# Kernel tuning notes

Measured on AMD Instinct MI355X. Metric: run time of the kernel, lower is better.

The kernel has to match this reference:

```python
import jax, jax.numpy as jnp
import numpy as np

NUM_HEADS = 16
KEY_DIM = 64
NUM_FEATURES = 256
D_MODEL = NUM_HEADS * KEY_DIM
EPS = 1e-6


def softmax_kernel(data, proj):
    # data: [..., N, D], proj: [D, F]
    # Faithful to source: ratio uses proj.shape[0] (=D), matching the TF code.
    data_normalizer = 1.0 / jnp.sqrt(jnp.sqrt(jnp.asarray(data.shape[-1], data.dtype)))
    ratio = 1.0 / jnp.sqrt(jnp.asarray(proj.shape[0], data.dtype))
    data = data_normalizer * data
    data_dash = jnp.einsum('...nd,df->...nf', data, proj)
    diag = jnp.sum(jnp.square(data), axis=-1, keepdims=True)  # [..., N, 1]
    return ratio * (jnp.exp(data_dash - diag / 2.0) + EPS)


def setup_inputs() -> dict:
    key = jax.random.key(0)
    ks = jax.random.split(key, 12)
    B, N = 4, 4096
    s = 1.0 / np.sqrt(D_MODEL)
    inp = {
        'queries': jax.random.normal(ks[0], (B, N, D_MODEL), jnp.float32),
        'keys': jax.random.normal(ks[1], (B, N, D_MODEL), jnp.float32),
        'Wq': jax.random.normal(ks[2], (D_MODEL, D_MODEL), jnp.float32) * s,
        'bq': jnp.zeros((D_MODEL,), jnp.float32),
        'Wk': jax.random.normal(ks[3], (D_MODEL, D_MODEL), jnp.float32) * s,
        'bk': jnp.zeros((D_MODEL,), jnp.float32),
        'Wv': jax.random.normal(ks[4], (D_MODEL, D_MODEL), jnp.float32) * s,
        'bv': jnp.zeros((D_MODEL,), jnp.float32),
        'Wo': jax.random.normal(ks[5], (D_MODEL, D_MODEL), jnp.float32) * s,
        'bo': jnp.zeros((D_MODEL,), jnp.float32),
        # GlorotNormal for [KEY_DIM, NUM_FEATURES]
        'proj': jax.random.normal(ks[6], (KEY_DIM, NUM_FEATURES), jnp.float32)
                * np.sqrt(2.0 / (KEY_DIM + NUM_FEATURES)),
    }
    return inp


def reference(queries, keys, Wq, bq, Wk, bk, Wv, bv, Wo, bo, proj):
    # Original code uses x = queries for q, k, v (self-attention); keys arg unused.
    x = queries
    B, N, _ = x.shape
    H, D = NUM_HEADS, KEY_DIM

    def split_heads(t):
        return t.reshape(B, N, H, D).transpose(0, 2, 1, 3)  # [B,H,N,D]

    q = split_heads(x @ Wq + bq)
    k = split_heads(x @ Wk + bk)
    v = split_heads(x @ Wv + bv)

    q_prime = softmax_kernel(q, proj)  # [B,H,N,F]
    k_prime = softmax_kernel(k, proj)  # [B,H,N,F]

    kv = jnp.einsum('bhnf,bhnd->bhfd', k_prime, v)        # [B,H,F,D]
    qkv = jnp.einsum('bhnf,bhfd->bhnd', q_prime, kv)       # [B,H,N,D]
    k_sum = jnp.sum(k_prime, axis=2)                        # [B,H,F]
    norm = jnp.einsum('bhnf,bhf->bhn', q_prime, k_sum) + EPS
    qkv = qkv / norm[..., None]

    out = qkv.transpose(0, 2, 1, 3).reshape(B, N, H * D)    # [B,N,d_model]
    return out @ Wo + bo
```

## Files before the change

### kernel.cpp

```cpp
#include <hip/hip_runtime.h>

typedef __attribute__((ext_vector_type(8))) short short8;
typedef __attribute__((ext_vector_type(4))) float f32x4;

#define MFMA16 __builtin_amdgcn_mfma_f32_16x16x32_bf16

#define GLOAD16(gp, lp) __builtin_amdgcn_global_load_lds(                      \
    (const __attribute__((address_space(1))) void*)(gp),                       \
    (__attribute__((address_space(3))) void*)(lp), 16, 0, 0)

__device__ __forceinline__ unsigned short f2bf(float f) {
  unsigned int u = __float_as_uint(f);
  unsigned int r = u + 0x7fffu + ((u >> 16) & 1u);
  return (unsigned short)(r >> 16);
}
__device__ __forceinline__ float bf2f(unsigned short h) {
  return __uint_as_float(((unsigned int)h) << 16);
}

__global__ __launch_bounds__(256) void cast_x_kernel(
    const float* __restrict__ in, unsigned short* __restrict__ out, int n4) {
  int i = blockIdx.x * 256 + threadIdx.x;
  if (i >= n4) return;
  float4 v = reinterpret_cast<const float4*>(in)[i];
  ushort4 o;
  o.x = f2bf(v.x); o.y = f2bf(v.y); o.z = f2bf(v.z); o.w = f2bf(v.w);
  reinterpret_cast<ushort4*>(out)[i] = o;
}

__global__ __launch_bounds__(256) void tcast_f32_kernel(
    const float* __restrict__ in, unsigned short* __restrict__ out, int R, int C) {
  __shared__ float t[64][65];
  int c0 = blockIdx.x * 64, r0 = blockIdx.y * 64;
  int tx = threadIdx.x, ty = threadIdx.y;
#pragma unroll
  for (int i = 0; i < 16; ++i)
    t[ty + 4 * i][tx] = in[(size_t)(r0 + ty + 4 * i) * C + c0 + tx];
  __syncthreads();
#pragma unroll
  for (int i = 0; i < 16; ++i)
    out[(size_t)(c0 + ty + 4 * i) * R + r0 + tx] = f2bf(t[tx][ty + 4 * i]);
}

__global__ __launch_bounds__(256) void tcast4_kernel(
    const float* __restrict__ i0, const float* __restrict__ i1,
    const float* __restrict__ i2, const float* __restrict__ i3,
    unsigned short* __restrict__ o0, unsigned short* __restrict__ o1,
    unsigned short* __restrict__ o2, unsigned short* __restrict__ o3) {
  const float* in = i0; unsigned short* out = o0;
  if (blockIdx.z == 1) { in = i1; out = o1; }
  else if (blockIdx.z == 2) { in = i2; out = o2; }
  else if (blockIdx.z == 3) { in = i3; out = o3; }
  __shared__ float t[64][65];
  int c0 = blockIdx.x * 64, r0 = blockIdx.y * 64;
  int tx = threadIdx.x, ty = threadIdx.y;
#pragma unroll
  for (int i = 0; i < 16; ++i)
    t[ty + 4 * i][tx] = in[(size_t)(r0 + ty + 4 * i) * 1024 + c0 + tx];
  __syncthreads();
#pragma unroll
  for (int i = 0; i < 16; ++i)
    out[(size_t)(c0 + ty + 4 * i) * 1024 + r0 + tx] = f2bf(t[tx][ty + 4 * i]);
}

template <int OUTF>
__global__ __launch_bounds__(256) void gemm_bt_kernel(
    const unsigned short* __restrict__ A,
    const unsigned short* W0, const unsigned short* W1, const unsigned short* W2,
    const float* b0, const float* b1, const float* b2,
    void* o0, void* o1, void* o2) {
  constexpr int KD = 1024, ND = 1024;
  const unsigned short* W = W0; const float* bias = b0; void* op = o0;
  if (blockIdx.z == 1) { W = W1; bias = b1; op = o1; }
  else if (blockIdx.z == 2) { W = W2; bias = b2; op = o2; }

  __shared__ unsigned short lsA[128 * 32];
  __shared__ unsigned short lsB[128 * 32];
  extern __shared__ unsigned short tt[];
  int tid = threadIdx.x;
  int w = tid >> 6, lane = tid & 63;
  int m0 = blockIdx.x * 128, n0 = blockIdx.y * 128;
  int wm = (w >> 1) * 64, wn = (w & 1) * 64;

  int srow0 = (w * 2 + 0) * 16 + (lane >> 2);
  int srow1 = (w * 2 + 1) * 16 + (lane >> 2);
  int scol = (lane & 3) * 8;
  const unsigned short* gA0 = A + (size_t)(m0 + srow0) * KD + scol;
  const unsigned short* gA1 = A + (size_t)(m0 + srow1) * KD + scol;
  const unsigned short* gB0 = W + (size_t)(n0 + srow0) * KD + scol;
  const unsigned short* gB1 = W + (size_t)(n0 + srow1) * KD + scol;
  unsigned short* lA0 = &lsA[(w * 2 + 0) * 512];
  unsigned short* lA1 = &lsA[(w * 2 + 1) * 512];
  unsigned short* lB0 = &lsB[(w * 2 + 0) * 512];
  unsigned short* lB1 = &lsB[(w * 2 + 1) * 512];

  f32x4 acc[4][4];
#pragma unroll
  for (int fm = 0; fm < 4; ++fm)
#pragma unroll
    for (int fn = 0; fn < 4; ++fn) acc[fm][fn] = (f32x4){0.f, 0.f, 0.f, 0.f};

  for (int kt = 0; kt < KD; kt += 32) {
    GLOAD16(gA0 + kt, lA0);
    GLOAD16(gA1 + kt, lA1);
    GLOAD16(gB0 + kt, lB0);
    GLOAD16(gB1 + kt, lB1);
    __syncthreads();
    short8 af[4], bfr[4];
#pragma unroll
    for (int fm = 0; fm < 4; ++fm)
      af[fm] = *reinterpret_cast<const short8*>(
          &lsA[(wm + fm * 16 + (lane & 15)) * 32 + (lane >> 4) * 8]);
#pragma unroll
    for (int fn = 0; fn < 4; ++fn)
      bfr[fn] = *reinterpret_cast<const short8*>(
          &lsB[(wn + fn * 16 + (lane & 15)) * 32 + (lane >> 4) * 8]);
#pragma unroll
    for (int fm = 0; fm < 4; ++fm)
#pragma unroll
      for (int fn = 0; fn < 4; ++fn)
        acc[fm][fn] = MFMA16(af[fm], bfr[fn], acc[fm][fn], 0, 0, 0);
    __syncthreads();
  }

  bool vpath = (OUTF == 3) && (blockIdx.z == 2);
#pragma unroll
  for (int fn = 0; fn < 4; ++fn) {
    int coll = wn + fn * 16 + (lane & 15);
    float bv = bias[n0 + coll];
#pragma unroll
    for (int fm = 0; fm < 4; ++fm) {
#pragma unroll
      for (int j = 0; j < 4; ++j) {
        int rowl = wm + fm * 16 + (lane >> 4) * 4 + j;
        float v = acc[fm][fn][j] + bv;
        if constexpr (OUTF == 1) {
          reinterpret_cast<float*>(op)[(size_t)(m0 + rowl) * ND + n0 + coll] = v;
        } else {
          if (vpath)
            tt[coll * 136 + rowl] = f2bf(v);
          else
            reinterpret_cast<unsigned short*>(op)[(size_t)(m0 + rowl) * ND + n0 + coll] =
                f2bf(v);
        }
      }
    }
  }
  if constexpr (OUTF == 3) {
    if (vpath) {
      __syncthreads();
      int b = m0 >> 12, tok0 = m0 & 4095;
      int c = tid >> 1, half = (tid & 1) * 64;
      unsigned short* dst = reinterpret_cast<unsigned short*>(op) +
                            (size_t)(b * 1024 + n0 + c) * 4096 + tok0 + half;
#pragma unroll
      for (int i = 0; i < 8; ++i) {
        short8 vv = *reinterpret_cast<const short8*>(&tt[c * 136 + half + i * 8]);
        *reinterpret_cast<short8*>(dst + i * 8) = vv;
      }
    }
  }
}

__global__ __launch_bounds__(256) void kv_fused_kernel(
    const unsigned short* __restrict__ K, const unsigned short* __restrict__ PT,
    const unsigned short* __restrict__ VT,
    float* __restrict__ kvp, float* __restrict__ ksp) {
  __shared__ unsigned short kp[256 * 40];
  int s = blockIdx.x, bh = blockIdx.y, b = bh >> 4, h = bh & 15;
  int tid = threadIdx.x, w = tid >> 6, lane = tid & 63;
  int lo = lane & 15, hi = lane >> 4;
  int f0w = w * 64;

  short8 pb[4][2];
#pragma unroll
  for (int fn = 0; fn < 4; ++fn) {
    int f = f0w + fn * 16 + lo;
    pb[fn][0] = *reinterpret_cast<const short8*>(PT + (size_t)f * 64 + hi * 8);
    pb[fn][1] = *reinterpret_cast<const short8*>(PT + (size_t)f * 64 + 32 + hi * 8);
  }
  const unsigned short* vbase[4];
#pragma unroll
  for (int fn = 0; fn < 4; ++fn)
    vbase[fn] = VT + (size_t)(bh * 64 + fn * 16 + lo) * 4096;

  f32x4 acck[4][4];
#pragma unroll
  for (int fm = 0; fm < 4; ++fm)
#pragma unroll
    for (int fn = 0; fn < 4; ++fn) acck[fm][fn] = (f32x4){0.f, 0.f, 0.f, 0.f};
  float ks[4] = {0.f, 0.f, 0.f, 0.f};

  for (int c = 0; c < 16; ++c) {
    int n0 = s * 512 + c * 32;
    const unsigned short* Ab = K + (size_t)(b * 4096 + n0) * 1024 + h * 64;
    short8 af[2][2], b2[4];
#pragma unroll
    for (int fm = 0; fm < 2; ++fm)
#pragma unroll
      for (int kt = 0; kt < 2; ++kt)
        af[fm][kt] = *reinterpret_cast<const short8*>(
            Ab + (size_t)(fm * 16 + lo) * 1024 + kt * 32 + hi * 8);
#pragma unroll
    for (int fn = 0; fn < 4; ++fn)
      b2[fn] = *reinterpret_cast<const short8*>(vbase[fn] + n0 + hi * 8);

    float dp[2] = {0.f, 0.f};
#pragma unroll
    for (int fm = 0; fm < 2; ++fm)
#pragma unroll
      for (int kt = 0; kt < 2; ++kt)
#pragma unroll
        for (int j = 0; j < 8; ++j) {
          float qv = bf2f((unsigned short)af[fm][kt][j]);
          dp[fm] += qv * qv;
        }
#pragma unroll
    for (int fm = 0; fm < 2; ++fm) {
      dp[fm] += __shfl_xor(dp[fm], 16);
      dp[fm] += __shfl_xor(dp[fm], 32);
    }
    f32x4 accf[2][4];
#pragma unroll
    for (int fm = 0; fm < 2; ++fm)
#pragma unroll
      for (int fn = 0; fn < 4; ++fn) accf[fm][fn] = (f32x4){0.f, 0.f, 0.f, 0.f};
#pragma unroll
    for (int fn = 0; fn < 4; ++fn) {
      accf[0][fn] = MFMA16(af[0][0], pb[fn][0], accf[0][fn], 0, 0, 0);
      accf[0][fn] = MFMA16(af[0][1], pb[fn][1], accf[0][fn], 0, 0, 0);
      accf[1][fn] = MFMA16(af[1][0], pb[fn][0], accf[1][fn], 0, 0, 0);
      accf[1][fn] = MFMA16(af[1][1], pb[fn][1], accf[1][fn], 0, 0, 0);
    }
#pragma unroll
    for (int fm = 0; fm < 2; ++fm)
#pragma unroll
      for (int fn = 0; fn < 4; ++fn) {
        ushort4 pk;
#pragma unroll
        for (int j = 0; j < 4; ++j) {
          float dg = __shfl(dp[fm], hi * 4 + j);
          float v = 0.125f *
                    (__expf(0.35355339059327373f * accf[fm][fn][j] - 0.0625f * dg) + 1e-6f);
          ks[fn] += v;
          ((unsigned short*)&pk)[j] = f2bf(v);
        }
        *reinterpret_cast<ushort4*>(&kp[(f0w + fn * 16 + lo) * 40 + fm * 16 + hi * 4]) = pk;
      }
    short8 a2[4];
#pragma unroll
    for (int fm = 0; fm < 4; ++fm)
      a2[fm] = *reinterpret_cast<const short8*>(&kp[(f0w + fm * 16 + lo) * 40 + hi * 8]);
#pragma unroll
    for (int fm = 0; fm < 4; ++fm)
#pragma unroll
      for (int fn = 0; fn < 4; ++fn)
        acck[fm][fn] = MFMA16(a2[fm], b2[fn], acck[fm][fn], 0, 0, 0);
  }
#pragma unroll
  for (int fn = 0; fn < 4; ++fn) {
    float v = ks[fn];
    v += __shfl_xor(v, 16);
    v += __shfl_xor(v, 32);
    if (hi == 0)
      ksp[(size_t)(s * 64 + bh) * 256 + f0w + fn * 16 + lo] = v;
  }
#pragma unroll
  for (int fm = 0; fm < 4; ++fm)
#pragma unroll
    for (int fn = 0; fn < 4; ++fn)
#pragma unroll
      for (int j = 0; j < 4; ++j)
        kvp[((size_t)(s * 64 + bh) * 256 + f0w + fm * 16 + hi * 4 + j) * 64 + fn * 16 + lo] =
            acck[fm][fn][j];
}

__global__ __launch_bounds__(256) void kvred_kernel(
    const float* __restrict__ kvp, const float* __restrict__ ksp,
    unsigned short* __restrict__ kvT, float* __restrict__ ksum) {
  __shared__ float t[64][65];
  int bh = blockIdx.x, g = blockIdx.y, tid = threadIdx.x;
  int fbase = g * 64;
  int fo = tid >> 2, dq = (tid & 3) * 16;
  float sum[16];
#pragma unroll
  for (int i = 0; i < 16; ++i) sum[i] = 0.f;
#pragma unroll
  for (int s = 0; s < 8; ++s) {
    const float* base = kvp + ((size_t)(s * 64 + bh) * 256 + fbase + fo) * 64 + dq;
#pragma unroll
    for (int i = 0; i < 16; ++i) sum[i] += base[i];
  }
#pragma unroll
  for (int i = 0; i < 16; ++i) t[fo][dq + i] = sum[i];
  __syncthreads();
  int d = tid >> 2, fq = (tid & 3) * 16;
  unsigned short wv[16];
#pragma unroll
  for (int i = 0; i < 16; ++i) wv[i] = f2bf(t[fq + i][d]);
  unsigned short* dst = kvT + (size_t)(bh * 64 + d) * 256 + fbase + fq;
  *reinterpret_cast<short8*>(dst) = *reinterpret_cast<const short8*>(&wv[0]);
  *reinterpret_cast<short8*>(dst + 8) = *reinterpret_cast<const short8*>(&wv[8]);
  if (g == 0) {
    float tsum = 0.f;
#pragma unroll
    for (int s = 0; s < 8; ++s) tsum += ksp[(size_t)(s * 64 + bh) * 256 + tid];
    ksum[bh * 256 + tid] = tsum;
  }
}

__global__ __launch_bounds__(256) void qkv_fused_kernel(
    const unsigned short* __restrict__ Q, const unsigned short* __restrict__ PT,
    const unsigned short* __restrict__ KVT, const float* __restrict__ KSUM,
    unsigned short* __restrict__ Y) {
  __shared__ unsigned short qp[128 * 128];
  int bh = blockIdx.y, b = bh >> 4, h = bh & 15;
  int t0 = blockIdx.x * 128;
  int tid = threadIdx.x, w = tid >> 6, lane = tid & 63;
  int lo = lane & 15, hi = lane >> 4;
  int r0 = w * 32;
  const unsigned short* Ab = Q + (size_t)(b * 4096 + t0 + r0) * 1024 + h * 64;

  float ksr[16];
#pragma unroll
  for (int fn = 0; fn < 16; ++fn) ksr[fn] = KSUM[bh * 256 + fn * 16 + lo];

  short8 af[2][2];
  float dp[2] = {0.f, 0.f};
#pragma unroll
  for (int fm = 0; fm < 2; ++fm)
#pragma unroll
    for (int kt = 0; kt < 2; ++kt) {
      af[fm][kt] = *reinterpret_cast<const short8*>(
          Ab + (size_t)(fm * 16 + lo) * 1024 + kt * 32 + hi * 8);
#pragma unroll
      for (int j = 0; j < 8; ++j) {
        float qv = bf2f((unsigned short)af[fm][kt][j]);
        dp[fm] += qv * qv;
      }
    }
#pragma unroll
  for (int fm = 0; fm < 2; ++fm) {
    dp[fm] += __shfl_xor(dp[fm], 16);
    dp[fm] += __shfl_xor(dp[fm], 32);
  }

  float np[2][4] = {{0.f, 0.f, 0.f, 0.f}, {0.f, 0.f, 0.f, 0.f}};
  f32x4 acco[2][4];
#pragma unroll
  for (int fm = 0; fm < 2; ++fm)
#pragma unroll
    for (int fn = 0; fn < 4; ++fn) acco[fm][fn] = (f32x4){0.f, 0.f, 0.f, 0.f};

#pragma unroll
  for (int hf = 0; hf < 2; ++hf) {
    f32x4 accf[2][8];
#pragma unroll
    for (int fm = 0; fm < 2; ++fm)
#pragma unroll
      for (int fn = 0; fn < 8; ++fn) accf[fm][fn] = (f32x4){0.f, 0.f, 0.f, 0.f};
#pragma unroll
    for (int fn = 0; fn < 8; ++fn) {
      int f = hf * 128 + fn * 16 + lo;
      short8 pb0 = *reinterpret_cast<const short8*>(PT + (size_t)f * 64 + hi * 8);
      short8 pb1 = *reinterpret_cast<const short8*>(PT + (size_t)f * 64 + 32 + hi * 8);
      accf[0][fn] = MFMA16(af[0][0], pb0, accf[0][fn], 0, 0, 0);
      accf[0][fn] = MFMA16(af[0][1], pb1, accf[0][fn], 0, 0, 0);
      accf[1][fn] = MFMA16(af[1][0], pb0, accf[1][fn], 0, 0, 0);
      accf[1][fn] = MFMA16(af[1][1], pb1, accf[1][fn], 0, 0, 0);
    }
#pragma unroll
    for (int fm = 0; fm < 2; ++fm)
#pragma unroll
      for (int fn = 0; fn < 8; ++fn)
#pragma unroll
        for (int j = 0; j < 4; ++j) {
          float dg = __shfl(dp[fm], hi * 4 + j);
          float v = 0.125f *
                    (__expf(0.35355339059327373f * accf[fm][fn][j] - 0.0625f * dg) + 1e-6f);
          np[fm][j] += v * ksr[hf * 8 + fn];
          int row = r0 + fm * 16 + hi * 4 + j;
          int fl = fn * 16 + lo;
          int byt = (row * 256 + fl * 2) ^ ((row & 7) << 4);
          *reinterpret_cast<unsigned short*>(reinterpret_cast<char*>(qp) + byt) = f2bf(v);
        }
#pragma unroll
    for (int kt2 = 0; kt2 < 4; ++kt2) {
      short8 a2[2], b2[4];
#pragma unroll
      for (int fm = 0; fm < 2; ++fm) {
        int row = r0 + fm * 16 + lo;
        int byt = (row * 256 + kt2 * 64 + hi * 16) ^ ((row & 7) << 4);
        a2[fm] = *reinterpret_cast<const short8*>(reinterpret_cast<char*>(qp) + byt);
      }
#pragma unroll
      for (int fn = 0; fn < 4; ++fn)
        b2[fn] = *reinterpret_cast<const short8*>(
            KVT + (size_t)(bh * 64 + fn * 16 + lo) * 256 + hf * 128 + kt2 * 32 + hi * 8);
#pragma unroll
      for (int fm = 0; fm < 2; ++fm)
#pragma unroll
        for (int fn = 0; fn < 4; ++fn)
          acco[fm][fn] = MFMA16(a2[fm], b2[fn], acco[fm][fn], 0, 0, 0);
    }
  }
#pragma unroll
  for (int fm = 0; fm < 2; ++fm)
#pragma unroll
    for (int j = 0; j < 4; ++j) {
      np[fm][j] += __shfl_xor(np[fm][j], 1);
      np[fm][j] += __shfl_xor(np[fm][j], 2);
      np[fm][j] += __shfl_xor(np[fm][j], 4);
      np[fm][j] += __shfl_xor(np[fm][j], 8);
    }
#pragma unroll
  for (int fm = 0; fm < 2; ++fm)
#pragma unroll
    for (int j = 0; j < 4; ++j) {
      float nv = np[fm][j] + 1e-6f;
      int row = b * 4096 + t0 + r0 + fm * 16 + hi * 4 + j;
#pragma unroll
      for (int fn = 0; fn < 4; ++fn)
        Y[(size_t)row * 1024 + h * 64 + fn * 16 + lo] = f2bf(acco[fm][fn][j] / nv);
    }
}

extern "C" void kernel_launch(void* const* d_in, const int* in_sizes, int n_in,
                              void* d_out, int out_size, void* d_ws, size_t ws_size,
                              hipStream_t stream) {
  (void)in_sizes; (void)n_in; (void)out_size; (void)ws_size;
  const float* x    = (const float*)d_in[0];
  const float* Wq   = (const float*)d_in[2];
  const float* bq   = (const float*)d_in[3];
  const float* Wk   = (const float*)d_in[4];
  const float* bk   = (const float*)d_in[5];
  const float* Wv   = (const float*)d_in[6];
  const float* bv   = (const float*)d_in[7];
  const float* Wo   = (const float*)d_in[8];
  const float* bo   = (const float*)d_in[9];
  const float* proj = (const float*)d_in[10];
  float* out = (float*)d_out;

  constexpr size_t SZ_XB = (size_t)16384 * 1024 * 2;
  constexpr size_t SZ_W  = (size_t)1024 * 1024 * 2;
  constexpr size_t SZ_PT = (size_t)256 * 64 * 2;

  char* p = (char*)d_ws;
  size_t off = 0;
  char* a_xb  = p + off; off += SZ_XB;
  char* a_WqT = p + off; off += SZ_W;
  char* a_WkT = p + off; off += SZ_W;
  char* a_WvT = p + off; off += SZ_W;
  char* a_WoT = p + off; off += SZ_W;
  char* a_pT  = p + off; off += SZ_PT;
  char* a_qb  = p + off; off += SZ_XB;
  char* a_kb  = p + off; off += SZ_XB;
  char* a_ksp  = p + off; off += (size_t)8 * 64 * 256 * 4;
  char* a_kvT  = p + off; off += (size_t)64 * 64 * 256 * 2;
  char* a_ksum = p + off; off += (size_t)64 * 256 * 4;

  char* a_kvp = a_xb;
  char* a_vT = (char*)d_out;
  char* a_y = a_kb;

  dim3 tb(64, 4);

  cast_x_kernel<<<16384, 256, 0, stream>>>(x, (unsigned short*)a_xb, 16384 * 1024 / 4);
  tcast4_kernel<<<dim3(16, 16, 4), tb, 0, stream>>>(
      Wq, Wk, Wv, Wo,
      (unsigned short*)a_WqT, (unsigned short*)a_WkT,
      (unsigned short*)a_WvT, (unsigned short*)a_WoT);
  tcast_f32_kernel<<<dim3(4, 1), tb, 0, stream>>>(proj, (unsigned short*)a_pT, 64, 256);

  gemm_bt_kernel<3><<<dim3(128, 8, 3), 256, 128 * 136 * 2, stream>>>(
      (unsigned short*)a_xb,
      (unsigned short*)a_WqT, (unsigned short*)a_WkT, (unsigned short*)a_WvT,
      bq, bk, bv, a_qb, a_kb, a_vT);

  kv_fused_kernel<<<dim3(8, 64), 256, 0, stream>>>(
      (unsigned short*)a_kb, (unsigned short*)a_pT, (unsigned short*)a_vT,
      (float*)a_kvp, (float*)a_ksp);
  kvred_kernel<<<dim3(64, 4), 256, 0, stream>>>(
      (float*)a_kvp, (float*)a_ksp, (unsigned short*)a_kvT, (float*)a_ksum);

  qkv_fused_kernel<<<dim3(32, 64), 256, 0, stream>>>(
      (unsigned short*)a_qb, (unsigned short*)a_pT, (unsigned short*)a_kvT,
      (float*)a_ksum, (unsigned short*)a_y);

  gemm_bt_kernel<1><<<dim3(128, 8, 1), 256, 0, stream>>>(
      (unsigned short*)a_y,
      (unsigned short*)a_WoT, nullptr, nullptr,
      bo, nullptr, nullptr, out, nullptr, nullptr);
}
```

Baseline: 342.3 us.

## Double GEMM K-step to 64 with XOR-swizzled LDS and shared epilogue buffer

After: 418.7 us. 1.22x slower.

```diff
diff --git a/kernel.cpp b/kernel.cpp
--- a/kernel.cpp
+++ b/kernel.cpp
@@ -74,25 +74,21 @@
   if (blockIdx.z == 1) { W = W1; bias = b1; op = o1; }
   else if (blockIdx.z == 2) { W = W2; bias = b2; op = o2; }
 
-  __shared__ unsigned short lsA[128 * 32];
-  __shared__ unsigned short lsB[128 * 32];
-  extern __shared__ unsigned short tt[];
+  __shared__ unsigned short smem[16384];
+  unsigned short* lsA = smem;
+  unsigned short* lsB = smem + 8192;
   int tid = threadIdx.x;
   int w = tid >> 6, lane = tid & 63;
+  int lo = lane & 15, hi = lane >> 4;
   int m0 = blockIdx.x * 128, n0 = blockIdx.y * 128;
   int wm = (w >> 1) * 64, wn = (w & 1) * 64;
 
-  int srow0 = (w * 2 + 0) * 16 + (lane >> 2);
-  int srow1 = (w * 2 + 1) * 16 + (lane >> 2);
-  int scol = (lane & 3) * 8;
-  const unsigned short* gA0 = A + (size_t)(m0 + srow0) * KD + scol;
-  const unsigned short* gA1 = A + (size_t)(m0 + srow1) * KD + scol;
-  const unsigned short* gB0 = W + (size_t)(n0 + srow0) * KD + scol;
-  const unsigned short* gB1 = W + (size_t)(n0 + srow1) * KD + scol;
-  unsigned short* lA0 = &lsA[(w * 2 + 0) * 512];
-  unsigned short* lA1 = &lsA[(w * 2 + 1) * 512];
-  unsigned short* lB0 = &lsB[(w * 2 + 0) * 512];
-  unsigned short* lB1 = &lsB[(w * 2 + 1) * 512];
+  int srow = w * 32 + (lane >> 3);
+  int sch = ((lane & 7) ^ (lane >> 3)) * 8;
+  const unsigned short* gA = A + (size_t)(m0 + srow) * KD + sch;
+  const unsigned short* gB = W + (size_t)(n0 + srow) * KD + sch;
+  unsigned short* lA = lsA + w * 2048;
+  unsigned short* lB = lsB + w * 2048;
 
   f32x4 acc[4][4];
 #pragma unroll
@@ -100,21 +96,36 @@
 #pragma unroll
     for (int fn = 0; fn < 4; ++fn) acc[fm][fn] = (f32x4){0.f, 0.f, 0.f, 0.f};
 
-  for (int kt = 0; kt < KD; kt += 32) {
-    GLOAD16(gA0 + kt, lA0);
-    GLOAD16(gA1 + kt, lA1);
-    GLOAD16(gB0 + kt, lB0);
-    GLOAD16(gB1 + kt, lB1);
+  int x7 = lo & 7;
+  for (int kt = 0; kt < KD; kt += 64) {
+#pragma unroll
+    for (int i = 0; i < 4; ++i) {
+      GLOAD16(gA + (size_t)i * 8 * KD + kt, lA + i * 512);
+      GLOAD16(gB + (size_t)i * 8 * KD + kt, lB + i * 512);
+    }
     __syncthreads();
     short8 af[4], bfr[4];
 #pragma unroll
     for (int fm = 0; fm < 4; ++fm)
       af[fm] = *reinterpret_cast<const short8*>(
-          &lsA[(wm + fm * 16 + (lane & 15)) * 32 + (lane >> 4) * 8]);
+          &lsA[(wm + fm * 16 + lo) * 64 + (hi ^ x7) * 8]);
 #pragma unroll
     for (int fn = 0; fn < 4; ++fn)
       bfr[fn] = *reinterpret_cast<const short8*>(
-          &lsB[(wn + fn * 16 + (lane & 15)) * 32 + (lane >> 4) * 8]);
+          &lsB[(wn + fn * 16 + lo) * 64 + (hi ^ x7) * 8]);
+#pragma unroll
+    for (int fm = 0; fm < 4; ++fm)
+#pragma unroll
+      for (int fn = 0; fn < 4; ++fn)
+        acc[fm][fn] = MFMA16(af[fm], bfr[fn], acc[fm][fn], 0, 0, 0);
+#pragma unroll
+    for (int fm = 0; fm < 4; ++fm)
+      af[fm] = *reinterpret_cast<const short8*>(
+          &lsA[(wm + fm * 16 + lo) * 64 + ((4 + hi) ^ x7) * 8]);
+#pragma unroll
+    for (int fn = 0; fn < 4; ++fn)
+      bfr[fn] = *reinterpret_cast<const short8*>(
+          &lsB[(wn + fn * 16 + lo) * 64 + ((4 + hi) ^ x7) * 8]);
 #pragma unroll
     for (int fm = 0; fm < 4; ++fm)
 #pragma unroll
@@ -124,40 +135,50 @@
   }
 
   bool vpath = (OUTF == 3) && (blockIdx.z == 2);
-#pragma unroll
-  for (int fn = 0; fn < 4; ++fn) {
-    int coll = wn + fn * 16 + (lane & 15);
-    float bv = bias[n0 + coll];
-#pragma unroll
-    for (int fm = 0; fm < 4; ++fm) {
-#pragma unroll
-      for (int j = 0; j < 4; ++j) {
-        int rowl = wm + fm * 16 + (lane >> 4) * 4 + j;
-        float v = acc[fm][fn][j] + bv;
-        if constexpr (OUTF == 1) {
-          reinterpret_cast<float*>(op)[(size_t)(m0 + rowl) * ND + n0 + coll] = v;
-        } else {
-          if (vpath)
-            tt[coll * 136 + rowl] = f2bf(v);
+  if (!vpath) {
+#pragma unroll
+    for (int fn = 0; fn < 4; ++fn) {
+      int coll = wn + fn * 16 + lo;
+      float bv = bias[n0 + coll];
+#pragma unroll
+      for (int fm = 0; fm < 4; ++fm) {
+#pragma unroll
+        for (int j = 0; j < 4; ++j) {
+          int rowl = wm + fm * 16 + hi * 4 + j;
+          float v = acc[fm][fn][j] + bv;
+          if constexpr (OUTF == 1)
+            reinterpret_cast<float*>(op)[(size_t)(m0 + rowl) * ND + n0 + coll] = v;
           else
             reinterpret_cast<unsigned short*>(op)[(size_t)(m0 + rowl) * ND + n0 + coll] =
                 f2bf(v);
         }
       }
     }
-  }
-  if constexpr (OUTF == 3) {
-    if (vpath) {
+  } else {
+    int b = m0 >> 12, tok0 = m0 & 4095;
+    int c2 = tid >> 2, q = (tid & 3) * 32;
+#pragma unroll
+    for (int half = 0; half < 2; ++half) {
       __syncthreads();
-      int b = m0 >> 12, tok0 = m0 & 4095;
-      int c = tid >> 1, half = (tid & 1) * 64;
+      if (wn == half * 64) {
+#pragma unroll
+        for (int fn = 0; fn < 4; ++fn) {
+          int c = fn * 16 + lo;
+          float bv = bias[n0 + half * 64 + c];
+#pragma unroll
+          for (int fm = 0; fm < 4; ++fm)
+#pragma unroll
+            for (int j = 0; j < 4; ++j)
+              smem[c * 136 + wm + fm * 16 + hi * 4 + j] = f2bf(acc[fm][fn][j] + bv);
+        }
+      }
+      __syncthreads();
       unsigned short* dst = reinterpret_cast<unsigned short*>(op) +
-                            (size_t)(b * 1024 + n0 + c) * 4096 + tok0 + half;
-#pragma unroll
-      for (int i = 0; i < 8; ++i) {
-        short8 vv = *reinterpret_cast<const short8*>(&tt[c * 136 + half + i * 8]);
-        *reinterpret_cast<short8*>(dst + i * 8) = vv;
-      }
+                            (size_t)(b * 1024 + n0 + half * 64 + c2) * 4096 + tok0 + q;
+#pragma unroll
+      for (int i = 0; i < 4; ++i)
+        *reinterpret_cast<short8*>(dst + i * 8) =
+            *reinterpret_cast<const short8*>(&smem[c2 * 136 + q + i * 8]);
     }
   }
 }
@@ -472,7 +493,7 @@
       (unsigned short*)a_WvT, (unsigned short*)a_WoT);
   tcast_f32_kernel<<<dim3(4, 1), tb, 0, stream>>>(proj, (unsigned short*)a_pT, 64, 256);
 
-  gemm_bt_kernel<3><<<dim3(128, 8, 3), 256, 128 * 136 * 2, stream>>>(
+  gemm_bt_kernel<3><<<dim3(128, 8, 3), 256, 0, stream>>>(
       (unsigned short*)a_xb,
       (unsigned short*)a_WqT, (unsigned short*)a_WkT, (unsigned short*)a_WvT,
       bq, bk, bv, a_qb, a_kb, a_vT);
```
